# Kernel optimization log

Measured on AMD Instinct MI355X. Metric: run time of the kernel, lower is better.

Reference implementation:

```python
import jax, jax.numpy as jnp
import numpy as np

STRICT_MAXIMA_BONUS = 10.0
EPS = 1e-7


def _shifter(x):
    # Edge-replicate pad by 1 in D,H,W (matches F.pad(..., 'replicate')).
    p = jnp.pad(x, ((0, 0), (0, 0), (1, 1), (1, 1), (1, 1)), mode='edge')
    D, H, W = x.shape[2:]
    def s(dd, dh, dw):
        return p[:, :, 1 + dd:1 + dd + D, 1 + dh:1 + dh + H, 1 + dw:1 + dw + W]
    return s


def setup_inputs() -> dict:
    key = jax.random.key(0)
    k1, k2 = jax.random.split(key)
    B, C, D, H, W = 2, 1, 4, 1024, 1024
    x = jax.random.normal(k1, (B, C, D, H, W), dtype=jnp.float32)
    # torch.rand(3,3).abs() noise added (scaled by eps) to every Hessian
    hes_noise = jax.random.uniform(k2, (3, 3), dtype=jnp.float32)
    return {"x": x, "hes_noise": hes_noise}


def _forward(x, hes_noise):
    B, C, D, H, W = x.shape
    s = _shifter(x)
    # --- first-order gradients (kornia spatial_gradient3d, mode='diff';
    #     kernel is depth-flipped before conv, hence gz sign) ---
    gx = 0.5 * (s(0, 0, 1) - s(0, 0, -1))   # d/dW
    gy = 0.5 * (s(0, 1, 0) - s(0, -1, 0))   # d/dH
    gz = 0.5 * (s(-1, 0, 0) - s(1, 0, 0))   # d/dD (depth-flipped kernel)
    b = jnp.stack([gx, gy, gz], axis=-1)     # (B,C,D,H,W,3)
    # --- second-order gradients ---
    dxx = s(0, 0, 1) - 2.0 * x + s(0, 0, -1)
    dyy = s(0, 1, 0) - 2.0 * x + s(0, -1, 0)
    dss = s(1, 0, 0) - 2.0 * x + s(-1, 0, 0)
    dxy = 0.25 * (s(0, -1, -1) - s(0, -1, 1) - s(0, 1, -1) + s(0, 1, 1))
    dys = 0.25 * (s(1, -1, 0) - s(1, 1, 0) - s(-1, -1, 0) + s(-1, 1, 0))
    dxs = 0.25 * (s(1, 0, -1) - s(1, 0, 1) - s(-1, 0, -1) + s(-1, 0, 1))
    Hes = jnp.stack([dxx, dxy, dxs,
                     dxy, dyy, dys,
                     dxs, dys, dss], axis=-1).reshape(B, C, D, H, W, 3, 3)
    Hes = Hes + hes_noise * EPS  # ill-conditioning guard, same noise per voxel
    # --- 3x3x3 strict NMS mask (max_pool3d k=3 s=1 p=1; pad identity = -inf) ---
    pooled = jax.lax.reduce_window(x, -jnp.inf, jax.lax.max,
                                   (1, 1, 3, 3, 3), (1, 1, 1, 1, 1), 'SAME')
    nms_mask = x == pooled
    # --- masked batched 3x3 solve: Hes @ x_solved = b at NMS positions only ---
    eye = jnp.eye(3, dtype=x.dtype)
    Hes_safe = jnp.where(nms_mask[..., None, None], Hes, eye)
    sol = jnp.linalg.solve(Hes_safe, b[..., None])[..., 0]
    x_solved = jnp.where(nms_mask[..., None], sol, 0.0)
    dx = -x_solved
    # discard refinements with offset magnitude > 0.7
    big = jnp.max(jnp.abs(dx), axis=-1, keepdims=True) > 0.7
    dx = jnp.where(big, 0.0, dx)
    # value refinement dy = 0.5 * b^T dx
    dy = 0.5 * jnp.sum(b * dx, axis=-1)
    y_max = x + dy + STRICT_MAXIMA_BONUS * nms_mask.astype(x.dtype)
    # coords: flip (x,y,z)->(d,h,w) channel order, add to integer grid
    dx_res = jnp.moveaxis(dx[..., ::-1], -1, 2)  # (B,C,3,D,H,W)
    gd = jnp.broadcast_to(jnp.arange(D, dtype=x.dtype)[:, None, None], (D, H, W))
    gh = jnp.broadcast_to(jnp.arange(H, dtype=x.dtype)[None, :, None], (D, H, W))
    gw = jnp.broadcast_to(jnp.arange(W, dtype=x.dtype)[None, None, :], (D, H, W))
    grid = jnp.stack([gd, gh, gw], axis=0)       # (3,D,H,W)
    coords_max = grid[None, None] + dx_res       # (B,C,3,D,H,W)
    return coords_max, y_max


def reference(x, hes_noise):
    return _forward(x, hes_noise)
```

## Files before the change

### kernel.cpp

```cpp
#include <hip/hip_runtime.h>

#define EPS_F 1e-7f
#define BONUS 10.0f

__global__ __launch_bounds__(256) void quadinterp3d_kernel(
    const float* __restrict__ x, const float* __restrict__ noise,
    float* __restrict__ out, int B, int D, int H, int W)
{
    int w = blockIdx.x * blockDim.x + threadIdx.x;
    int h = blockIdx.y;
    int bd = blockIdx.z;
    int d = bd % D;
    int b = bd / D;
    if (w >= W) return;

    const long long HW  = (long long)H * W;
    const long long DHW = (long long)D * HW;

    int wm = max(w - 1, 0), wp = min(w + 1, W - 1);
    int hm = max(h - 1, 0), hp = min(h + 1, H - 1);
    int dm = max(d - 1, 0), dp = min(d + 1, D - 1);

    const float* base = x + (long long)b * DHW;

    int ds[3] = {dm, d, dp};
    int hs[3] = {hm, h, hp};
    int wsx[3] = {wm, w, wp};

    float v[3][3][3];
#pragma unroll
    for (int i = 0; i < 3; ++i) {
#pragma unroll
        for (int j = 0; j < 3; ++j) {
            const float* row = base + (long long)ds[i] * HW + (long long)hs[j] * W;
#pragma unroll
            for (int k = 0; k < 3; ++k) v[i][j][k] = row[wsx[k]];
        }
    }

    float c = v[1][1][1];

    float gx = 0.5f * (v[1][1][2] - v[1][1][0]);
    float gy = 0.5f * (v[1][2][1] - v[1][0][1]);
    float gz = 0.5f * (v[0][1][1] - v[2][1][1]);

    float dxx = v[1][1][2] - 2.0f * c + v[1][1][0];
    float dyy = v[1][2][1] - 2.0f * c + v[1][0][1];
    float dss = v[2][1][1] - 2.0f * c + v[0][1][1];
    float dxy = 0.25f * (v[1][0][0] - v[1][0][2] - v[1][2][0] + v[1][2][2]);
    float dys = 0.25f * (v[2][0][1] - v[2][2][1] - v[0][0][1] + v[0][2][1]);
    float dxs = 0.25f * (v[2][1][0] - v[2][1][2] - v[0][1][0] + v[0][1][2]);

    float mx27 = c;
#pragma unroll
    for (int i = 0; i < 3; ++i)
#pragma unroll
        for (int j = 0; j < 3; ++j)
#pragma unroll
            for (int k = 0; k < 3; ++k) mx27 = fmaxf(mx27, v[i][j][k]);
    bool mask = (c == mx27);

    float dx0 = 0.0f, dx1 = 0.0f, dx2 = 0.0f, dy = 0.0f;

    if (mask) {
        float A[3][3];
        float rhs[3];
        A[0][0] = dxx + noise[0] * EPS_F;
        A[0][1] = dxy + noise[1] * EPS_F;
        A[0][2] = dxs + noise[2] * EPS_F;
        A[1][0] = dxy + noise[3] * EPS_F;
        A[1][1] = dyy + noise[4] * EPS_F;
        A[1][2] = dys + noise[5] * EPS_F;
        A[2][0] = dxs + noise[6] * EPS_F;
        A[2][1] = dys + noise[7] * EPS_F;
        A[2][2] = dss + noise[8] * EPS_F;
        rhs[0] = gx; rhs[1] = gy; rhs[2] = gz;

        {
            int p = 0; float am = fabsf(A[0][0]);
            if (fabsf(A[1][0]) > am) { am = fabsf(A[1][0]); p = 1; }
            if (fabsf(A[2][0]) > am) { p = 2; }
            if (p != 0) {
#pragma unroll
                for (int j = 0; j < 3; ++j) { float t = A[0][j]; A[0][j] = A[p][j]; A[p][j] = t; }
                float t = rhs[0]; rhs[0] = rhs[p]; rhs[p] = t;
            }
            float m1 = A[1][0] / A[0][0];
            float m2 = A[2][0] / A[0][0];
            A[1][1] -= m1 * A[0][1]; A[1][2] -= m1 * A[0][2]; rhs[1] -= m1 * rhs[0];
            A[2][1] -= m2 * A[0][1]; A[2][2] -= m2 * A[0][2]; rhs[2] -= m2 * rhs[0];
        }
        {
            if (fabsf(A[2][1]) > fabsf(A[1][1])) {
                float t;
                t = A[1][1]; A[1][1] = A[2][1]; A[2][1] = t;
                t = A[1][2]; A[1][2] = A[2][2]; A[2][2] = t;
                t = rhs[1]; rhs[1] = rhs[2]; rhs[2] = t;
            }
            float m = A[2][1] / A[1][1];
            A[2][2] -= m * A[1][2]; rhs[2] -= m * rhs[1];
        }
        float s2 = rhs[2] / A[2][2];
        float s1 = (rhs[1] - A[1][2] * s2) / A[1][1];
        float s0 = (rhs[0] - A[0][1] * s1 - A[0][2] * s2) / A[0][0];

        dx0 = -s0; dx1 = -s1; dx2 = -s2;
        float amax = fmaxf(fabsf(dx0), fmaxf(fabsf(dx1), fabsf(dx2)));
        if (amax > 0.7f) { dx0 = 0.0f; dx1 = 0.0f; dx2 = 0.0f; }
        dy = 0.5f * (gx * dx0 + gy * dx1 + gz * dx2);
    }

    long long spatial = (long long)d * HW + (long long)h * W + w;
    float* oc = out + (long long)b * 3 * DHW + spatial;
    oc[0]       = (float)d + dx2;
    oc[DHW]     = (float)h + dx1;
    oc[2 * DHW] = (float)w + dx0;
    float* oy = out + (long long)B * 3 * DHW + (long long)b * DHW + spatial;
    oy[0] = c + dy + (mask ? BONUS : 0.0f);
}

extern "C" void kernel_launch(void* const* d_in, const int* in_sizes, int n_in,
                              void* d_out, int out_size, void* d_ws, size_t ws_size,
                              hipStream_t stream) {
    const float* x     = (const float*)d_in[0];
    const float* noise = (const float*)d_in[1];
    float* out = (float*)d_out;

    const int B = 2, D = 4, H = 1024, W = 1024;

    dim3 block(256, 1, 1);
    dim3 grid(W / 256, H, B * D);
    quadinterp3d_kernel<<<grid, block, 0, stream>>>(x, noise, out, B, D, H, W);
}
```

Baseline: 184.0 us.

## Process four voxels per thread with vectorized loads and nontemporal vector stores

Each thread now handles four consecutive W positions, loading a 6-wide window per row (a float4 plus two edge scalars) and reusing it across the four stencils. Outputs are written as float4 nontemporal stores, and the grid shrinks by a factor of four. The aim is fewer redundant loads and wider memory transactions. In exchange, register pressure rises and the number of launched threads drops to 16K per slice, which lowers parallelism.

```diff
diff --git a/kernel.cpp b/kernel.cpp
--- a/kernel.cpp
+++ b/kernel.cpp
@@ -3,120 +3,139 @@
 #define EPS_F 1e-7f
 #define BONUS 10.0f
 
+typedef float v4f __attribute__((ext_vector_type(4)));
+
 __global__ __launch_bounds__(256) void quadinterp3d_kernel(
     const float* __restrict__ x, const float* __restrict__ noise,
     float* __restrict__ out, int B, int D, int H, int W)
 {
-    int w = blockIdx.x * blockDim.x + threadIdx.x;
-    int h = blockIdx.y;
-    int bd = blockIdx.z;
-    int d = bd % D;
-    int b = bd / D;
-    if (w >= W) return;
+    const int t  = threadIdx.x;
+    const int w0 = (blockIdx.x * 256 + t) * 4;
+    const int h  = blockIdx.y;
+    const int bd = blockIdx.z;
+    const int d  = bd % D;
+    const int b  = bd / D;
+    if (w0 >= W) return;
 
     const long long HW  = (long long)H * W;
     const long long DHW = (long long)D * HW;
 
-    int wm = max(w - 1, 0), wp = min(w + 1, W - 1);
-    int hm = max(h - 1, 0), hp = min(h + 1, H - 1);
-    int dm = max(d - 1, 0), dp = min(d + 1, D - 1);
+    const int hm = max(h - 1, 0), hp = min(h + 1, H - 1);
+    const int dm = max(d - 1, 0), dp = min(d + 1, D - 1);
+    const int wl = (w0 == 0) ? 0 : w0 - 1;
+    const int wr = (w0 + 4 >= W) ? W - 1 : w0 + 4;
 
     const float* base = x + (long long)b * DHW;
+    const int ds[3] = {dm, d, dp};
+    const int hs[3] = {hm, h, hp};
 
-    int ds[3] = {dm, d, dp};
-    int hs[3] = {hm, h, hp};
-    int wsx[3] = {wm, w, wp};
-
-    float v[3][3][3];
+    float r[9][6];
 #pragma unroll
     for (int i = 0; i < 3; ++i) {
 #pragma unroll
         for (int j = 0; j < 3; ++j) {
             const float* row = base + (long long)ds[i] * HW + (long long)hs[j] * W;
-#pragma unroll
-            for (int k = 0; k < 3; ++k) v[i][j][k] = row[wsx[k]];
+            v4f v4 = *(const v4f*)(row + w0);
+            float* m = r[i * 3 + j];
+            m[0] = row[wl];
+            m[1] = v4.x; m[2] = v4.y; m[3] = v4.z; m[4] = v4.w;
+            m[5] = row[wr];
         }
     }
 
-    float c = v[1][1][1];
+    float n0 = noise[0], n1 = noise[1], n2 = noise[2];
+    float n3 = noise[3], n4 = noise[4], n5 = noise[5];
+    float n6 = noise[6], n7 = noise[7], n8 = noise[8];
 
-    float gx = 0.5f * (v[1][1][2] - v[1][1][0]);
-    float gy = 0.5f * (v[1][2][1] - v[1][0][1]);
-    float gz = 0.5f * (v[0][1][1] - v[2][1][1]);
+    v4f od, oh, ow, oy;
+    float* pod = (float*)&od; float* poh = (float*)&oh;
+    float* pow_ = (float*)&ow; float* poy = (float*)&oy;
 
-    float dxx = v[1][1][2] - 2.0f * c + v[1][1][0];
-    float dyy = v[1][2][1] - 2.0f * c + v[1][0][1];
-    float dss = v[2][1][1] - 2.0f * c + v[0][1][1];
-    float dxy = 0.25f * (v[1][0][0] - v[1][0][2] - v[1][2][0] + v[1][2][2]);
-    float dys = 0.25f * (v[2][0][1] - v[2][2][1] - v[0][0][1] + v[0][2][1]);
-    float dxs = 0.25f * (v[2][1][0] - v[2][1][2] - v[0][1][0] + v[0][1][2]);
+#pragma unroll
+    for (int k = 0; k < 4; ++k) {
+        float c = r[4][k + 1];
 
-    float mx27 = c;
+        float gx = 0.5f * (r[4][k + 2] - r[4][k]);
+        float gy = 0.5f * (r[5][k + 1] - r[3][k + 1]);
+        float gz = 0.5f * (r[1][k + 1] - r[7][k + 1]);
+
+        float dxx = r[4][k + 2] - 2.0f * c + r[4][k];
+        float dyy = r[5][k + 1] - 2.0f * c + r[3][k + 1];
+        float dss = r[7][k + 1] - 2.0f * c + r[1][k + 1];
+        float dxy = 0.25f * (r[3][k] - r[3][k + 2] - r[5][k] + r[5][k + 2]);
+        float dys = 0.25f * (r[6][k + 1] - r[8][k + 1] - r[0][k + 1] + r[2][k + 1]);
+        float dxs = 0.25f * (r[7][k] - r[7][k + 2] - r[1][k] + r[1][k + 2]);
+
+        float mx = c;
 #pragma unroll
-    for (int i = 0; i < 3; ++i)
+        for (int q = 0; q < 9; ++q) {
+            mx = fmaxf(mx, r[q][k]);
+            mx = fmaxf(mx, r[q][k + 1]);
+            mx = fmaxf(mx, r[q][k + 2]);
+        }
+        bool mask = (c == mx);
+
+        float dx0 = 0.0f, dx1 = 0.0f, dx2 = 0.0f, dy = 0.0f;
+        if (mask) {
+            float A[3][3], rhs[3];
+            A[0][0] = dxx + n0 * EPS_F;
+            A[0][1] = dxy + n1 * EPS_F;
+            A[0][2] = dxs + n2 * EPS_F;
+            A[1][0] = dxy + n3 * EPS_F;
+            A[1][1] = dyy + n4 * EPS_F;
+            A[1][2] = dys + n5 * EPS_F;
+            A[2][0] = dxs + n6 * EPS_F;
+            A[2][1] = dys + n7 * EPS_F;
+            A[2][2] = dss + n8 * EPS_F;
+            rhs[0] = gx; rhs[1] = gy; rhs[2] = gz;
+
+            {
+                int p = 0; float am = fabsf(A[0][0]);
+                if (fabsf(A[1][0]) > am) { am = fabsf(A[1][0]); p = 1; }
+                if (fabsf(A[2][0]) > am) { p = 2; }
+                if (p != 0) {
 #pragma unroll
-        for (int j = 0; j < 3; ++j)
-#pragma unroll
-            for (int k = 0; k < 3; ++k) mx27 = fmaxf(mx27, v[i][j][k]);
-    bool mask = (c == mx27);
+                    for (int j = 0; j < 3; ++j) { float tt = A[0][j]; A[0][j] = A[p][j]; A[p][j] = tt; }
+                    float tt = rhs[0]; rhs[0] = rhs[p]; rhs[p] = tt;
+                }
+                float m1 = A[1][0] / A[0][0];
+                float m2 = A[2][0] / A[0][0];
+                A[1][1] -= m1 * A[0][1]; A[1][2] -= m1 * A[0][2]; rhs[1] -= m1 * rhs[0];
+                A[2][1] -= m2 * A[0][1]; A[2][2] -= m2 * A[0][2]; rhs[2] -= m2 * rhs[0];
+            }
+            {
+                if (fabsf(A[2][1]) > fabsf(A[1][1])) {
+                    float tt;
+                    tt = A[1][1]; A[1][1] = A[2][1]; A[2][1] = tt;
+                    tt = A[1][2]; A[1][2] = A[2][2]; A[2][2] = tt;
+                    tt = rhs[1]; rhs[1] = rhs[2]; rhs[2] = tt;
+                }
+                float m = A[2][1] / A[1][1];
+                A[2][2] -= m * A[1][2]; rhs[2] -= m * rhs[1];
+            }
+            float s2 = rhs[2] / A[2][2];
+            float s1 = (rhs[1] - A[1][2] * s2) / A[1][1];
+            float s0 = (rhs[0] - A[0][1] * s1 - A[0][2] * s2) / A[0][0];
 
-    float dx0 = 0.0f, dx1 = 0.0f, dx2 = 0.0f, dy = 0.0f;
+            dx0 = -s0; dx1 = -s1; dx2 = -s2;
+            float amax = fmaxf(fabsf(dx0), fmaxf(fabsf(dx1), fabsf(dx2)));
+            if (amax > 0.7f) { dx0 = 0.0f; dx1 = 0.0f; dx2 = 0.0f; }
+            dy = 0.5f * (gx * dx0 + gy * dx1 + gz * dx2);
+        }
 
-    if (mask) {
-        float A[3][3];
-        float rhs[3];
-        A[0][0] = dxx + noise[0] * EPS_F;
-        A[0][1] = dxy + noise[1] * EPS_F;
-        A[0][2] = dxs + noise[2] * EPS_F;
-        A[1][0] = dxy + noise[3] * EPS_F;
-        A[1][1] = dyy + noise[4] * EPS_F;
-        A[1][2] = dys + noise[5] * EPS_F;
-        A[2][0] = dxs + noise[6] * EPS_F;
-        A[2][1] = dys + noise[7] * EPS_F;
-        A[2][2] = dss + noise[8] * EPS_F;
-        rhs[0] = gx; rhs[1] = gy; rhs[2] = gz;
-
-        {
-            int p = 0; float am = fabsf(A[0][0]);
-            if (fabsf(A[1][0]) > am) { am = fabsf(A[1][0]); p = 1; }
-            if (fabsf(A[2][0]) > am) { p = 2; }
-            if (p != 0) {
-#pragma unroll
-                for (int j = 0; j < 3; ++j) { float t = A[0][j]; A[0][j] = A[p][j]; A[p][j] = t; }
-                float t = rhs[0]; rhs[0] = rhs[p]; rhs[p] = t;
-            }
-            float m1 = A[1][0] / A[0][0];
-            float m2 = A[2][0] / A[0][0];
-            A[1][1] -= m1 * A[0][1]; A[1][2] -= m1 * A[0][2]; rhs[1] -= m1 * rhs[0];
-            A[2][1] -= m2 * A[0][1]; A[2][2] -= m2 * A[0][2]; rhs[2] -= m2 * rhs[0];
-        }
-        {
-            if (fabsf(A[2][1]) > fabsf(A[1][1])) {
-                float t;
-                t = A[1][1]; A[1][1] = A[2][1]; A[2][1] = t;
-                t = A[1][2]; A[1][2] = A[2][2]; A[2][2] = t;
-                t = rhs[1]; rhs[1] = rhs[2]; rhs[2] = t;
-            }
-            float m = A[2][1] / A[1][1];
-            A[2][2] -= m * A[1][2]; rhs[2] -= m * rhs[1];
-        }
-        float s2 = rhs[2] / A[2][2];
-        float s1 = (rhs[1] - A[1][2] * s2) / A[1][1];
-        float s0 = (rhs[0] - A[0][1] * s1 - A[0][2] * s2) / A[0][0];
-
-        dx0 = -s0; dx1 = -s1; dx2 = -s2;
-        float amax = fmaxf(fabsf(dx0), fmaxf(fabsf(dx1), fabsf(dx2)));
-        if (amax > 0.7f) { dx0 = 0.0f; dx1 = 0.0f; dx2 = 0.0f; }
-        dy = 0.5f * (gx * dx0 + gy * dx1 + gz * dx2);
+        pod[k] = (float)d + dx2;
+        poh[k] = (float)h + dx1;
+        pow_[k] = (float)(w0 + k) + dx0;
+        poy[k] = c + dy + (mask ? BONUS : 0.0f);
     }
 
-    long long spatial = (long long)d * HW + (long long)h * W + w;
+    const long long spatial = (long long)d * HW + (long long)h * W + w0;
     float* oc = out + (long long)b * 3 * DHW + spatial;
-    oc[0]       = (float)d + dx2;
-    oc[DHW]     = (float)h + dx1;
-    oc[2 * DHW] = (float)w + dx0;
-    float* oy = out + (long long)B * 3 * DHW + (long long)b * DHW + spatial;
-    oy[0] = c + dy + (mask ? BONUS : 0.0f);
+    __builtin_nontemporal_store(od, (v4f*)(oc));
+    __builtin_nontemporal_store(oh, (v4f*)(oc + DHW));
+    __builtin_nontemporal_store(ow, (v4f*)(oc + 2 * DHW));
+    float* oyp = out + (long long)B * 3 * DHW + (long long)b * DHW + spatial;
+    __builtin_nontemporal_store(oy, (v4f*)(oyp));
 }
 
 extern "C" void kernel_launch(void* const* d_in, const int* in_sizes, int n_in,
@@ -129,6 +148,6 @@
     const int B = 2, D = 4, H = 1024, W = 1024;
 
     dim3 block(256, 1, 1);
-    dim3 grid(W / 256, H, B * D);
+    dim3 grid(W / (256 * 4), H, B * D);
     quadinterp3d_kernel<<<grid, block, 0, stream>>>(x, noise, out, B, D, H, W);
 }
```

New measurement: 187.9 us. 1.02x slower.
